# Performance work log

Measured on AMD Instinct MI355X. Metric: run time of the kernel, lower is better.

## Reference

```python
import jax, jax.numpy as jnp
import numpy as np

M = 8192
A_N, A_K = 64, 64  # out_factors[0], in_factors[0]
B_N, B_K = 64, 64  # out_factors[1], in_factors[1]
K = A_K * B_K
N = A_N * B_N


def setup_inputs() -> dict:
    key = jax.random.key(0)
    kx, ka, kb, kbias = jax.random.split(key, 4)
    x = jax.random.normal(kx, (M, K), dtype=jnp.float32)
    A = jax.random.normal(ka, (A_N, A_K), dtype=jnp.float32) * (1.0 / np.sqrt(A_K))
    B = jax.random.normal(kb, (B_N, B_K), dtype=jnp.float32) * (1.0 / np.sqrt(B_K))
    bias = jax.random.normal(kbias, (N,), dtype=jnp.float32) * 0.01
    return {"x": x, "A": A, "B": B, "bias": bias}


def reference(x, A, B, bias):
    # Y = X @ (A kron B)^T + bias, computed without materializing A kron B.
    # Column index n of the kron weight decomposes as n = p*B_N + q with
    # (A kron B)[n, k] = A[p, k//B_K] * B[q, k%B_K].
    m, k = x.shape
    a_n, a_k = A.shape
    b_n, b_k = B.shape
    xr = x.reshape(m, a_k, b_k)                    # [M, A_K, B_K]
    y = jnp.einsum('mab,qb->maq', xr, B)           # contract B factor
    y = jnp.einsum('maq,pa->mpq', y, A)            # contract A factor
    return y.reshape(m, a_n * b_n) + bias[None, :]
```

## Files before the change

kernel.cpp:

```cpp
#include <hip/hip_runtime.h>

typedef __attribute__((ext_vector_type(8))) short short8v;
typedef __attribute__((ext_vector_type(4))) short short4v;
typedef __attribute__((ext_vector_type(4))) float float4v;

__device__ __forceinline__ short f2bf(float f) {
  __bf16 h = (__bf16)f;
  return __builtin_bit_cast(short, h);
}

__device__ __forceinline__ short8v load_frag8(const float* __restrict__ p) {
  float4 a = *reinterpret_cast<const float4*>(p);
  float4 b = *reinterpret_cast<const float4*>(p + 4);
  short8v r;
  r[0] = f2bf(a.x); r[1] = f2bf(a.y); r[2] = f2bf(a.z); r[3] = f2bf(a.w);
  r[4] = f2bf(b.x); r[5] = f2bf(b.y); r[6] = f2bf(b.z); r[7] = f2bf(b.w);
  return r;
}

__device__ __forceinline__ void stage_weight(const float* __restrict__ src,
                                             short* __restrict__ dst, int tid) {
  const int r = tid >> 2;
  const int c0 = (tid & 3) << 4;
  const float* p = src + r * 64 + c0;
  float4 f0 = reinterpret_cast<const float4*>(p)[0];
  float4 f1 = reinterpret_cast<const float4*>(p)[1];
  float4 f2 = reinterpret_cast<const float4*>(p)[2];
  float4 f3 = reinterpret_cast<const float4*>(p)[3];
  short8v g0, g1;
  g0[0] = f2bf(f0.x); g0[1] = f2bf(f0.y); g0[2] = f2bf(f0.z); g0[3] = f2bf(f0.w);
  g0[4] = f2bf(f1.x); g0[5] = f2bf(f1.y); g0[6] = f2bf(f1.z); g0[7] = f2bf(f1.w);
  g1[0] = f2bf(f2.x); g1[1] = f2bf(f2.y); g1[2] = f2bf(f2.z); g1[3] = f2bf(f2.w);
  g1[4] = f2bf(f3.x); g1[5] = f2bf(f3.y); g1[6] = f2bf(f3.z); g1[7] = f2bf(f3.w);
  const int sw = (r & 7) << 3;
  *reinterpret_cast<short8v*>(&dst[r * 64 + ((c0)     ^ sw)]) = g0;
  *reinterpret_cast<short8v*>(&dst[r * 64 + ((c0 + 8) ^ sw)]) = g1;
}

__global__ __launch_bounds__(256, 3)
void kron64_kernel(const float* __restrict__ x, const float* __restrict__ A,
                   const float* __restrict__ B, const float* __restrict__ bias,
                   float* __restrict__ out) {
  __shared__ short bw[4096];
  __shared__ short aw[4096];
  __shared__ short y1[4][2048];

  const int tid = threadIdx.x;
  const int w = tid >> 6;
  const int lane = tid & 63;
  const int g = lane >> 4;
  const int c = lane & 15;
  const int swz = (c & 7) << 3;

  stage_weight(B, bw, tid);
  stage_weight(A, aw, tid);
  __syncthreads();

  const int m = blockIdx.x * 4 + w;
  const float* xm = x + (size_t)m * 4096;
  float* om = out + (size_t)m * 4096;
  short* yw = y1[w];
  const float4v vzero = {0.f, 0.f, 0.f, 0.f};

  short4v pk[4][2];
  {
    short8v bfr[4][2];
#pragma unroll
    for (int qt = 0; qt < 4; ++qt)
#pragma unroll
      for (int kk = 0; kk < 2; ++kk)
        bfr[qt][kk] = *reinterpret_cast<const short8v*>(
            &bw[(16 * qt + c) * 64 + ((32 * kk + 8 * g) ^ swz)]);

#pragma unroll
    for (int at = 0; at < 4; ++at) {
      float4v acc[4];
#pragma unroll
      for (int qt = 0; qt < 4; ++qt) acc[qt] = vzero;
#pragma unroll
      for (int kk = 0; kk < 2; ++kk) {
        short8v xfrag = load_frag8(xm + (16 * at + c) * 64 + 32 * kk + 8 * g);
#pragma unroll
        for (int qt = 0; qt < 4; ++qt)
          acc[qt] = __builtin_amdgcn_mfma_f32_16x16x32_bf16(
              xfrag, bfr[qt][kk], acc[qt], 0, 0, 0);
      }
#pragma unroll
      for (int qt = 0; qt < 4; ++qt) {
        short4v v;
        v[0] = f2bf(acc[qt][0]); v[1] = f2bf(acc[qt][1]);
        v[2] = f2bf(acc[qt][2]); v[3] = f2bf(acc[qt][3]);
        if (qt < 2) {
          int idx = ((16 * qt + c) * 64 + 16 * at + 4 * g) ^ swz;
          *reinterpret_cast<short4v*>(&yw[idx]) = v;
        } else {
          pk[at][qt - 2] = v;
        }
      }
    }
  }

#pragma unroll
  for (int h = 0; h < 2; ++h) {
    if (h == 1) {
#pragma unroll
      for (int at = 0; at < 4; ++at)
#pragma unroll
        for (int q2 = 0; q2 < 2; ++q2) {
          int idx = ((16 * q2 + c) * 64 + 16 * at + 4 * g) ^ swz;
          *reinterpret_cast<short4v*>(&yw[idx]) = pk[at][q2];
        }
    }
    __asm__ volatile("s_waitcnt lgkmcnt(0)" ::: "memory");

    short8v yfr[2][2];
#pragma unroll
    for (int qtl = 0; qtl < 2; ++qtl)
#pragma unroll
      for (int kk = 0; kk < 2; ++kk) {
        int idx = (((16 * qtl + c) * 64) + ((32 * kk + 8 * g) ^ swz));
        yfr[qtl][kk] = *reinterpret_cast<const short8v*>(&yw[idx]);
      }

#pragma unroll
    for (int pt = 0; pt < 4; ++pt) {
      short8v afr[2];
#pragma unroll
      for (int kk = 0; kk < 2; ++kk)
        afr[kk] = *reinterpret_cast<const short8v*>(
            &aw[(16 * pt + c) * 64 + ((32 * kk + 8 * g) ^ swz)]);
#pragma unroll
      for (int qtl = 0; qtl < 2; ++qtl) {
        const int n = (16 * pt + c) * 64 + 16 * (2 * h + qtl) + 4 * g;
        float4 bv = *reinterpret_cast<const float4*>(bias + n);
        float4v acc; acc[0] = bv.x; acc[1] = bv.y; acc[2] = bv.z; acc[3] = bv.w;
#pragma unroll
        for (int kk = 0; kk < 2; ++kk)
          acc = __builtin_amdgcn_mfma_f32_16x16x32_bf16(
              yfr[qtl][kk], afr[kk], acc, 0, 0, 0);
        *reinterpret_cast<float4v*>(om + n) = acc;
      }
    }
  }
}

extern "C" void kernel_launch(void* const* d_in, const int* in_sizes, int n_in,
                              void* d_out, int out_size, void* d_ws, size_t ws_size,
                              hipStream_t stream) {
  (void)in_sizes; (void)n_in; (void)out_size; (void)d_ws; (void)ws_size;
  const float* x    = (const float*)d_in[0];
  const float* A    = (const float*)d_in[1];
  const float* B    = (const float*)d_in[2];
  const float* bias = (const float*)d_in[3];
  float* out = (float*)d_out;

  dim3 grid(2048), block(256);
  hipLaunchKernelGGL(kron64_kernel, grid, block, 0, stream, x, A, B, bias, out);
}
```

Before: 57.52 us.

## Process four rows per wave with double-buffered register prefetch of x

Each wave now handles four output rows instead of one, and the grid shrinks from 2048 to 512 blocks. Loads of x are issued one half-row ahead into two register buffers, so global loads overlap the first-stage MFMAs. The intermediate buffer grows to a full 64x64 bf16 tile per wave, which replaces the register stash of half the result. The weight staging and B-fragment loads are amortized over more rows. In exchange, shared memory and register use rise and occupancy drops to 2 blocks per SIMD, with fewer blocks available to cover the GPU.

```diff
diff --git a/kernel.cpp b/kernel.cpp
--- a/kernel.cpp
+++ b/kernel.cpp
@@ -9,9 +9,7 @@
   return __builtin_bit_cast(short, h);
 }
 
-__device__ __forceinline__ short8v load_frag8(const float* __restrict__ p) {
-  float4 a = *reinterpret_cast<const float4*>(p);
-  float4 b = *reinterpret_cast<const float4*>(p + 4);
+__device__ __forceinline__ short8v cvt8(float4 a, float4 b) {
   short8v r;
   r[0] = f2bf(a.x); r[1] = f2bf(a.y); r[2] = f2bf(a.z); r[3] = f2bf(a.w);
   r[4] = f2bf(b.x); r[5] = f2bf(b.y); r[6] = f2bf(b.z); r[7] = f2bf(b.w);
@@ -27,23 +25,21 @@
   float4 f1 = reinterpret_cast<const float4*>(p)[1];
   float4 f2 = reinterpret_cast<const float4*>(p)[2];
   float4 f3 = reinterpret_cast<const float4*>(p)[3];
-  short8v g0, g1;
-  g0[0] = f2bf(f0.x); g0[1] = f2bf(f0.y); g0[2] = f2bf(f0.z); g0[3] = f2bf(f0.w);
-  g0[4] = f2bf(f1.x); g0[5] = f2bf(f1.y); g0[6] = f2bf(f1.z); g0[7] = f2bf(f1.w);
-  g1[0] = f2bf(f2.x); g1[1] = f2bf(f2.y); g1[2] = f2bf(f2.z); g1[3] = f2bf(f2.w);
-  g1[4] = f2bf(f3.x); g1[5] = f2bf(f3.y); g1[6] = f2bf(f3.z); g1[7] = f2bf(f3.w);
+  short8v g0 = cvt8(f0, f1), g1 = cvt8(f2, f3);
   const int sw = (r & 7) << 3;
   *reinterpret_cast<short8v*>(&dst[r * 64 + ((c0)     ^ sw)]) = g0;
   *reinterpret_cast<short8v*>(&dst[r * 64 + ((c0 + 8) ^ sw)]) = g1;
 }
 
-__global__ __launch_bounds__(256, 3)
+constexpr int ROWS = 4;
+
+__global__ __launch_bounds__(256, 2)
 void kron64_kernel(const float* __restrict__ x, const float* __restrict__ A,
                    const float* __restrict__ B, const float* __restrict__ bias,
                    float* __restrict__ out) {
   __shared__ short bw[4096];
   __shared__ short aw[4096];
-  __shared__ short y1[4][2048];
+  __shared__ short y1[4][4096];
 
   const int tid = threadIdx.x;
   const int w = tid >> 6;
@@ -56,89 +52,98 @@
   stage_weight(A, aw, tid);
   __syncthreads();
 
-  const int m = blockIdx.x * 4 + w;
-  const float* xm = x + (size_t)m * 4096;
-  float* om = out + (size_t)m * 4096;
+  const int m0 = (blockIdx.x * 4 + w) * ROWS;
+  const float* xm = x + (size_t)m0 * 4096;
   short* yw = y1[w];
   const float4v vzero = {0.f, 0.f, 0.f, 0.f};
 
-  short4v pk[4][2];
-  {
-    short8v bfr[4][2];
+  short8v bfr[4][2];
 #pragma unroll
-    for (int qt = 0; qt < 4; ++qt)
+  for (int qt = 0; qt < 4; ++qt)
 #pragma unroll
-      for (int kk = 0; kk < 2; ++kk)
-        bfr[qt][kk] = *reinterpret_cast<const short8v*>(
-            &bw[(16 * qt + c) * 64 + ((32 * kk + 8 * g) ^ swz)]);
+    for (int kk = 0; kk < 2; ++kk)
+      bfr[qt][kk] = *reinterpret_cast<const short8v*>(
+          &bw[(16 * qt + c) * 64 + ((32 * kk + 8 * g) ^ swz)]);
+
+  float4 xa[8], xb[8];
+
+  auto issue = [&](float4* buf, int H) {
+    const float* p0 =
+        xm + (size_t)(H >> 1) * 4096 + ((H & 1) * 32 + c) * 64 + 8 * g;
+#pragma unroll
+    for (int atl = 0; atl < 2; ++atl)
+#pragma unroll
+      for (int kk = 0; kk < 2; ++kk) {
+        const float* p = p0 + atl * 1024 + kk * 32;
+        buf[(atl * 2 + kk) * 2 + 0] = reinterpret_cast<const float4*>(p)[0];
+        buf[(atl * 2 + kk) * 2 + 1] = reinterpret_cast<const float4*>(p)[1];
+      }
+  };
+
+  issue(xa, 0);
+  issue(xb, 1);
 
 #pragma unroll
-    for (int at = 0; at < 4; ++at) {
-      float4v acc[4];
+  for (int r = 0; r < ROWS; ++r) {
 #pragma unroll
-      for (int qt = 0; qt < 4; ++qt) acc[qt] = vzero;
+    for (int h = 0; h < 2; ++h) {
+      const int H = 2 * r + h;
+      float4* cur = (H & 1) ? xb : xa;
 #pragma unroll
-      for (int kk = 0; kk < 2; ++kk) {
-        short8v xfrag = load_frag8(xm + (16 * at + c) * 64 + 32 * kk + 8 * g);
+      for (int atl = 0; atl < 2; ++atl) {
+        const int at = 2 * h + atl;
+        float4v acc[4];
 #pragma unroll
-        for (int qt = 0; qt < 4; ++qt)
-          acc[qt] = __builtin_amdgcn_mfma_f32_16x16x32_bf16(
-              xfrag, bfr[qt][kk], acc[qt], 0, 0, 0);
-      }
+        for (int qt = 0; qt < 4; ++qt) acc[qt] = vzero;
 #pragma unroll
-      for (int qt = 0; qt < 4; ++qt) {
-        short4v v;
-        v[0] = f2bf(acc[qt][0]); v[1] = f2bf(acc[qt][1]);
-        v[2] = f2bf(acc[qt][2]); v[3] = f2bf(acc[qt][3]);
-        if (qt < 2) {
+        for (int kk = 0; kk < 2; ++kk) {
+          short8v xf = cvt8(cur[(atl * 2 + kk) * 2], cur[(atl * 2 + kk) * 2 + 1]);
+#pragma unroll
+          for (int qt = 0; qt < 4; ++qt)
+            acc[qt] = __builtin_amdgcn_mfma_f32_16x16x32_bf16(
+                xf, bfr[qt][kk], acc[qt], 0, 0, 0);
+        }
+#pragma unroll
+        for (int qt = 0; qt < 4; ++qt) {
+          short4v v;
+          v[0] = f2bf(acc[qt][0]); v[1] = f2bf(acc[qt][1]);
+          v[2] = f2bf(acc[qt][2]); v[3] = f2bf(acc[qt][3]);
           int idx = ((16 * qt + c) * 64 + 16 * at + 4 * g) ^ swz;
           *reinterpret_cast<short4v*>(&yw[idx]) = v;
-        } else {
-          pk[at][qt - 2] = v;
         }
       }
+      if (H + 2 < 2 * ROWS) issue(cur, H + 2);
     }
-  }
 
+    float* om = out + (size_t)(m0 + r) * 4096;
 #pragma unroll
-  for (int h = 0; h < 2; ++h) {
-    if (h == 1) {
+    for (int qh = 0; qh < 2; ++qh) {
+      short8v yfr[2][2];
 #pragma unroll
-      for (int at = 0; at < 4; ++at)
+      for (int qtl = 0; qtl < 2; ++qtl)
 #pragma unroll
-        for (int q2 = 0; q2 < 2; ++q2) {
-          int idx = ((16 * q2 + c) * 64 + 16 * at + 4 * g) ^ swz;
-          *reinterpret_cast<short4v*>(&yw[idx]) = pk[at][q2];
+        for (int kk = 0; kk < 2; ++kk) {
+          int idx = ((16 * (2 * qh + qtl) + c) * 64) + ((32 * kk + 8 * g) ^ swz);
+          yfr[qtl][kk] = *reinterpret_cast<const short8v*>(&yw[idx]);
         }
-    }
-    __asm__ volatile("s_waitcnt lgkmcnt(0)" ::: "memory");
-
-    short8v yfr[2][2];
 #pragma unroll
-    for (int qtl = 0; qtl < 2; ++qtl)
-#pragma unroll
-      for (int kk = 0; kk < 2; ++kk) {
-        int idx = (((16 * qtl + c) * 64) + ((32 * kk + 8 * g) ^ swz));
-        yfr[qtl][kk] = *reinterpret_cast<const short8v*>(&yw[idx]);
-      }
-
-#pragma unroll
-    for (int pt = 0; pt < 4; ++pt) {
-      short8v afr[2];
-#pragma unroll
-      for (int kk = 0; kk < 2; ++kk)
-        afr[kk] = *reinterpret_cast<const short8v*>(
-            &aw[(16 * pt + c) * 64 + ((32 * kk + 8 * g) ^ swz)]);
-#pragma unroll
-      for (int qtl = 0; qtl < 2; ++qtl) {
-        const int n = (16 * pt + c) * 64 + 16 * (2 * h + qtl) + 4 * g;
-        float4 bv = *reinterpret_cast<const float4*>(bias + n);
-        float4v acc; acc[0] = bv.x; acc[1] = bv.y; acc[2] = bv.z; acc[3] = bv.w;
+      for (int pt = 0; pt < 4; ++pt) {
+        short8v afr[2];
 #pragma unroll
         for (int kk = 0; kk < 2; ++kk)
-          acc = __builtin_amdgcn_mfma_f32_16x16x32_bf16(
-              yfr[qtl][kk], afr[kk], acc, 0, 0, 0);
-        *reinterpret_cast<float4v*>(om + n) = acc;
+          afr[kk] = *reinterpret_cast<const short8v*>(
+              &aw[(16 * pt + c) * 64 + ((32 * kk + 8 * g) ^ swz)]);
+#pragma unroll
+        for (int qtl = 0; qtl < 2; ++qtl) {
+          const int n = (16 * pt + c) * 64 + 16 * (2 * qh + qtl) + 4 * g;
+          float4 bv = *reinterpret_cast<const float4*>(bias + n);
+          float4v acc; acc[0] = bv.x; acc[1] = bv.y; acc[2] = bv.z; acc[3] = bv.w;
+#pragma unroll
+          for (int kk = 0; kk < 2; ++kk)
+            acc = __builtin_amdgcn_mfma_f32_16x16x32_bf16(
+                yfr[qtl][kk], afr[kk], acc, 0, 0, 0);
+          *reinterpret_cast<float4v*>(om + n) = acc;
+        }
       }
     }
   }
@@ -154,6 +159,6 @@
   const float* bias = (const float*)d_in[3];
   float* out = (float*)d_out;
 
-  dim3 grid(2048), block(256);
+  dim3 grid(512), block(256);
   hipLaunchKernelGGL(kron64_kernel, grid, block, 0, stream, x, A, B, bias, out);
 }
```

New measurement: 78.88 us. 1.37x slower.
